# Kernel tuning notes

Measured on AMD Instinct MI355X. Metric: run time of the kernel, lower is better.

## Reference

```python
import jax, jax.numpy as jnp
import numpy as np

N = 50000        # nodes
E = 1_600_000    # edges per graph (avg degree 32)
T = 5            # timesteps per node
F_RAW = 395      # 3 meta channels + 392 signal
H_GRU = 64
HID = 40


def setup_inputs() -> dict:
    key = jax.random.key(0)
    ks = jax.random.split(key, 20)
    s = 0.05
    inp = {
        "x": jax.random.normal(ks[0], (N, T, F_RAW), jnp.float32),
        "edge_index": jax.random.randint(ks[1], (2, E), 0, N, dtype=jnp.int32),
        "feat_edge_index": jax.random.randint(ks[2], (2, E), 0, N, dtype=jnp.int32),
        # FeatureCNN: Conv1d(1, 16, kernel_size=40, stride=88) -> L=5 -> flatten 80
        "conv_w": jax.random.normal(ks[3], (16, 1, 40), jnp.float32) * s,
        "conv_b": jnp.zeros((16,), jnp.float32),
        "lin1_w": jax.random.normal(ks[4], (40, 80), jnp.float32) * s,
        "lin1_b": jnp.zeros((40,), jnp.float32),
        # GRU(input=41, hidden=64), PyTorch gate order: r, z, n
        "gru_w_ih": jax.random.normal(ks[5], (3 * H_GRU, 41), jnp.float32) * s,
        "gru_w_hh": jax.random.normal(ks[6], (3 * H_GRU, H_GRU), jnp.float32) * s,
        "gru_b_ih": jnp.zeros((3 * H_GRU,), jnp.float32),
        "gru_b_hh": jnp.zeros((3 * H_GRU,), jnp.float32),
        "gcn1_w": jax.random.normal(ks[7], (104, HID), jnp.float32) * s,
        "gcn1_b": jnp.zeros((HID,), jnp.float32),
        "gcn2_w": jax.random.normal(ks[8], (104, HID), jnp.float32) * s,
        "gcn2_b": jnp.zeros((HID,), jnp.float32),
        "mlp_w": jax.random.normal(ks[9], (1, 2 * HID), jnp.float32) * s,
        "mlp_b": jnp.zeros((1,), jnp.float32),
    }
    return inp


def _gcn(h_in, ei, W, b):
    """GCNConv: sym-normalized sum aggregation with self-loops."""
    n = h_in.shape[0]
    h = h_in @ W                                   # [n, out]
    loops = jnp.arange(n, dtype=ei.dtype)
    src = jnp.concatenate([ei[0], loops])
    dst = jnp.concatenate([ei[1], loops])
    deg = jax.ops.segment_sum(jnp.ones_like(dst, h.dtype), dst, num_segments=n)
    dinv = jax.lax.rsqrt(jnp.maximum(deg, 1.0))    # deg >= 1 due to self-loops
    norm = dinv[src] * dinv[dst]                   # [E+n]
    msg = h[src] * norm[:, None]                   # gather + scale
    return jax.ops.segment_sum(msg, dst, num_segments=n) + b


def _cnn_gru(x, conv_w, conv_b, lin1_w, lin1_b, gru_w_ih, gru_w_hh, gru_b_ih, gru_b_hh):
    n = x.shape[0]
    y = x[:, :, 2].reshape(-1, 1)                  # [n*5, 1]
    sig = x[:, :, 3:].reshape(-1, 1, 392)          # [n*5, 1, 392]
    # FeatureCNN: conv1d k=40 s=88 -> [n*5, 16, 5] -> relu -> flatten 80
    c = jax.lax.conv_general_dilated(
        sig, conv_w, window_strides=(88,), padding="VALID",
        dimension_numbers=("NCH", "OIH", "NCH"))
    c = jax.nn.relu(c + conv_b[None, :, None]).reshape(-1, 80)
    out = jax.nn.relu(c @ lin1_w.T + lin1_b)       # [n*5, 40]
    seq = jnp.concatenate([out, y], axis=1).reshape(n, 5, 41)

    def gru_step(h, xt):
        gi = xt @ gru_w_ih.T + gru_b_ih            # [n, 192]
        gh = h @ gru_w_hh.T + gru_b_hh
        ir, iz, inn = jnp.split(gi, 3, axis=1)
        hr, hz, hn_ = jnp.split(gh, 3, axis=1)
        r = jax.nn.sigmoid(ir + hr)
        z = jax.nn.sigmoid(iz + hz)
        ng = jnp.tanh(inn + r * hn_)
        h = (1.0 - z) * ng + z * h
        return h, None

    h0 = jnp.zeros((n, H_GRU), x.dtype)
    hn, _ = jax.lax.scan(gru_step, h0, jnp.swapaxes(seq[:, :4, :], 0, 1))
    return jnp.concatenate([seq[:, 4, :-1], hn], axis=1)  # [n, 104]


def reference(x, edge_index, feat_edge_index, conv_w, conv_b, lin1_w, lin1_b,
              gru_w_ih, gru_w_hh, gru_b_ih, gru_b_hh,
              gcn1_w, gcn1_b, gcn2_w, gcn2_b, mlp_w, mlp_b):
    feats = _cnn_gru(x, conv_w, conv_b, lin1_w, lin1_b,
                     gru_w_ih, gru_w_hh, gru_b_ih, gru_b_hh)   # [N, 104]
    emb1 = jax.nn.relu(_gcn(feats, edge_index, gcn1_w, gcn1_b))      # [N, 40]
    emb2 = jax.nn.relu(_gcn(feats, feat_edge_index, gcn2_w, gcn2_b)) # [N, 40]
    emb = jnp.concatenate([emb1, emb2], axis=1)                      # [N, 80]
    return emb @ mlp_w.T + mlp_b                                     # [N, 1]
```

## Files before the change

kernel.cpp:

```cpp
#include <hip/hip_runtime.h>
#include <hip/hip_fp16.h>
#include <math.h>


#define NB      512
#define MAXNPB  104
#define PART_T  4096
#define GN      96

__global__ __launch_bounds__(512) void k_cnn(
    const float* __restrict__ x,
    const float* __restrict__ conv_w,
    const float* __restrict__ conv_b,
    const float* __restrict__ lin_w,
    const float* __restrict__ lin_b,
    float* __restrict__ seq,
    float* __restrict__ feats,
    int nrows, int nnodes)
{
    __shared__ __align__(16) float smem[64 * 200];
    __shared__ __align__(16) float s_cw[16][44];
    __shared__ __align__(16) float s_lw[40][84];
    __shared__ float s_cb[16];
    __shared__ float s_lb[40];

    const int tid = threadIdx.x;
    const int r0  = blockIdx.x * 64;

    float sg[25];
    #pragma unroll
    for (int it = 0; it < 25; ++it) {
        int i = tid + it * 512;
        int row = i / 200, e = i - row * 200;
        int p = e / 40, kk = e - p * 40;
        int gr = r0 + row; if (gr >= nrows) gr = nrows - 1;
        sg[it] = x[(size_t)gr * 395 + 3 + 88 * p + kk];
    }

    for (int i = tid; i < 640;  i += 512) s_cw[i / 40][i % 40] = conv_w[i];
    for (int i = tid; i < 3200; i += 512) s_lw[i / 80][i % 80] = lin_w[i];
    if (tid < 16) s_cb[tid] = conv_b[tid];
    if (tid >= 64 && tid < 104) s_lb[tid - 64] = lin_b[tid - 64];

    if (tid < 64) {
        int gr = r0 + tid;
        if (gr < nrows) {
            float y = x[(size_t)gr * 395 + 2];
            int node = gr / 5, t = gr - node * 5;
            if (t < 4) seq[(t * nnodes + node) * 41 + 40] = y;
        }
    }

    #pragma unroll
    for (int it = 0; it < 25; ++it) {
        int i = tid + it * 512;
        int row = i / 200, e = i - row * 200;
        smem[row * 200 + e] = sg[it];
    }
    __syncthreads();

    const int row = tid >> 3, cg = tid & 7;
    float creg[2][5];
    {
        float acc[2][5];
        #pragma unroll
        for (int cc = 0; cc < 2; ++cc) {
            float b = s_cb[2 * cg + cc];
            #pragma unroll
            for (int p = 0; p < 5; ++p) acc[cc][p] = b;
        }
        #pragma unroll
        for (int k4 = 0; k4 < 40; k4 += 4) {
            float4 sv[5];
            #pragma unroll
            for (int p = 0; p < 5; ++p)
                sv[p] = *(const float4*)&smem[row * 200 + p * 40 + k4];
            #pragma unroll
            for (int cc = 0; cc < 2; ++cc) {
                float4 w4 = *(const float4*)&s_cw[2 * cg + cc][k4];
                #pragma unroll
                for (int p = 0; p < 5; ++p)
                    acc[cc][p] += w4.x * sv[p].x + w4.y * sv[p].y + w4.z * sv[p].z + w4.w * sv[p].w;
            }
        }
        #pragma unroll
        for (int cc = 0; cc < 2; ++cc)
            #pragma unroll
            for (int p = 0; p < 5; ++p) creg[cc][p] = fmaxf(acc[cc][p], 0.0f);
    }
    __syncthreads();

    #pragma unroll
    for (int cc = 0; cc < 2; ++cc)
        #pragma unroll
        for (int p = 0; p < 5; ++p)
            smem[row * 84 + (2 * cg + cc) * 5 + p] = creg[cc][p];
    __syncthreads();

    {
        const int jg = tid & 7;
        float acc[5];
        #pragma unroll
        for (int jj = 0; jj < 5; ++jj) acc[jj] = s_lb[5 * jg + jj];
        #pragma unroll
        for (int i4 = 0; i4 < 80; i4 += 4) {
            float4 c0 = *(const float4*)&smem[row * 84 + i4];
            #pragma unroll
            for (int jj = 0; jj < 5; ++jj) {
                float4 w4 = *(const float4*)&s_lw[5 * jg + jj][i4];
                acc[jj] += w4.x * c0.x + w4.y * c0.y + w4.z * c0.z + w4.w * c0.w;
            }
        }
        int gr = r0 + row;
        if (gr < nrows) {
            int node = gr / 5, t = gr - node * 5;
            #pragma unroll
            for (int jj = 0; jj < 5; ++jj) {
                float v = fmaxf(acc[jj], 0.0f);
                if (t < 4) seq[(t * nnodes + node) * 41 + 5 * jg + jj] = v;
                else       feats[node * 104 + 5 * jg + jj] = v;
            }
        }
    }
}

__global__ __launch_bounds__(512) void k_gru(
    const float* __restrict__ seq,
    const float* __restrict__ w_ih,
    const float* __restrict__ w_hh,
    const float* __restrict__ b_ih,
    const float* __restrict__ b_hh,
    float* __restrict__ feats,
    int nnodes)
{
    __shared__ __align__(16) __half s_wi[41][192];
    __shared__ __align__(16) __half s_wh[64][192];
    __shared__ __align__(16) float  s_h[64][104];
    __shared__ __align__(16) __half s_x[41][104];
    __shared__ float s_bi[192], s_bh[192];

    const int tid  = threadIdx.x;
    const int nblk = blockIdx.x * GN;

    float xr[8];
    #pragma unroll
    for (int r = 0; r < 8; ++r) {
        int i = tid + r * 512;
        if (i < GN * 41) {
            int nl = i / 41, k = i - nl * 41;
            int node = nblk + nl; if (node >= nnodes) node = nnodes - 1;
            xr[r] = seq[(size_t)node * 41 + k];
        }
    }

    for (int i = tid; i < 192 * 41; i += 512) { int g = i / 41, k = i - g * 41; s_wi[k][g] = __float2half(w_ih[i]); }
    for (int i = tid; i < 192 * 64; i += 512) { int g = i >> 6,  k = i & 63;    s_wh[k][g] = __float2half(w_hh[i]); }
    if (tid < 192) { s_bi[tid] = b_ih[tid]; s_bh[tid] = b_hh[tid]; }
    for (int i = tid; i < 64 * 104; i += 512) ((float*)s_h)[i] = 0.0f;

    #pragma unroll
    for (int r = 0; r < 8; ++r) {
        int i = tid + r * 512;
        if (i < GN * 41) { int nl = i / 41, k = i - nl * 41; s_x[k][nl] = __float2half(xr[r]); }
    }
    __syncthreads();

    const int jg = tid & 31, ngp = tid >> 5;
    const int j0 = 2 * jg, n0 = 6 * ngp;

    float hreg[2][6];
    #pragma unroll
    for (int a = 0; a < 2; ++a)
        #pragma unroll
        for (int b = 0; b < 6; ++b) hreg[a][b] = 0.0f;

    for (int t = 0; t < 4; ++t) {
        if (t < 3) {
            #pragma unroll
            for (int r = 0; r < 8; ++r) {
                int i = tid + r * 512;
                if (i < GN * 41) {
                    int nl = i / 41, k = i - nl * 41;
                    int node = nblk + nl; if (node >= nnodes) node = nnodes - 1;
                    xr[r] = seq[(size_t)((t + 1) * nnodes + node) * 41 + k];
                }
            }
        }

        float ar[2][6], az[2][6], ani[2][6], anh[2][6];
        #pragma unroll
        for (int a = 0; a < 2; ++a)
            #pragma unroll
            for (int b = 0; b < 6; ++b) { ar[a][b]=0.f; az[a][b]=0.f; ani[a][b]=0.f; anh[a][b]=0.f; }

        for (int k = 0; k < 41; ++k) {
            float2 x01 = __half22float2(*(const __half2*)&s_x[k][n0]);
            float2 x23 = __half22float2(*(const __half2*)&s_x[k][n0 + 2]);
            float2 x45 = __half22float2(*(const __half2*)&s_x[k][n0 + 4]);
            float xv[6] = {x01.x, x01.y, x23.x, x23.y, x45.x, x45.y};
            float2 wr = __half22float2(*(const __half2*)&s_wi[k][j0]);
            float2 wz = __half22float2(*(const __half2*)&s_wi[k][64 + j0]);
            float2 wn = __half22float2(*(const __half2*)&s_wi[k][128 + j0]);
            #pragma unroll
            for (int nn = 0; nn < 6; ++nn) {
                ar[0][nn] += wr.x*xv[nn]; ar[1][nn] += wr.y*xv[nn];
                az[0][nn] += wz.x*xv[nn]; az[1][nn] += wz.y*xv[nn];
                ani[0][nn]+= wn.x*xv[nn]; ani[1][nn]+= wn.y*xv[nn];
            }
        }
        for (int k = 0; k < 64; ++k) {
            float2 h01 = *(const float2*)&s_h[k][n0];
            float2 h23 = *(const float2*)&s_h[k][n0 + 2];
            float2 h45 = *(const float2*)&s_h[k][n0 + 4];
            float hv[6] = {h01.x, h01.y, h23.x, h23.y, h45.x, h45.y};
            float2 wr = __half22float2(*(const __half2*)&s_wh[k][j0]);
            float2 wz = __half22float2(*(const __half2*)&s_wh[k][64 + j0]);
            float2 wn = __half22float2(*(const __half2*)&s_wh[k][128 + j0]);
            #pragma unroll
            for (int nn = 0; nn < 6; ++nn) {
                ar[0][nn] += wr.x*hv[nn]; ar[1][nn] += wr.y*hv[nn];
                az[0][nn] += wz.x*hv[nn]; az[1][nn] += wz.y*hv[nn];
                anh[0][nn]+= wn.x*hv[nn]; anh[1][nn]+= wn.y*hv[nn];
            }
        }

        #pragma unroll
        for (int jj = 0; jj < 2; ++jj) {
            int j = j0 + jj;
            float br  = s_bi[j]      + s_bh[j];
            float bz  = s_bi[64 + j] + s_bh[64 + j];
            float bin = s_bi[128 + j], bhn = s_bh[128 + j];
            #pragma unroll
            for (int nn = 0; nn < 6; ++nn) {
                float r = 1.0f / (1.0f + expf(-(ar[jj][nn] + br)));
                float z = 1.0f / (1.0f + expf(-(az[jj][nn] + bz)));
                float g = tanhf(ani[jj][nn] + bin + r * (anh[jj][nn] + bhn));
                hreg[jj][nn] = (1.0f - z) * g + z * hreg[jj][nn];
            }
        }
        __syncthreads();

        if (t < 3) {
            #pragma unroll
            for (int jj = 0; jj < 2; ++jj) {
                *(float2*)&s_h[j0 + jj][n0]     = make_float2(hreg[jj][0], hreg[jj][1]);
                *(float2*)&s_h[j0 + jj][n0 + 2] = make_float2(hreg[jj][2], hreg[jj][3]);
                *(float2*)&s_h[j0 + jj][n0 + 4] = make_float2(hreg[jj][4], hreg[jj][5]);
            }
            #pragma unroll
            for (int r = 0; r < 8; ++r) {
                int i = tid + r * 512;
                if (i < GN * 41) { int nl = i / 41, k = i - nl * 41; s_x[k][nl] = __float2half(xr[r]); }
            }
            __syncthreads();
        }
    }

    #pragma unroll
    for (int jj = 0; jj < 2; ++jj)
        #pragma unroll
        for (int nn = 0; nn < 6; ++nn) {
            int node = nblk + n0 + nn;
            if (node < nnodes) feats[node * 104 + 40 + j0 + jj] = hreg[jj][nn];
        }
}

__global__ __launch_bounds__(256) void k_hw(
    const float* __restrict__ feats,
    const float* __restrict__ w1,
    const float* __restrict__ w2,
    const float* __restrict__ dinv1,
    const float* __restrict__ dinv2,
    __half* __restrict__ hs1,
    __half* __restrict__ hs2,
    int nnodes)
{
    __shared__ __align__(16) float s_f[128][108];
    __shared__ __align__(16) float s_w[80][108];
    __shared__ float s_d[2][128];

    const int tid  = threadIdx.x;
    const int nblk = blockIdx.x * 128;

    for (int i = tid; i < 128 * 104; i += 256) {
        int n = i / 104, k = i - n * 104;
        int node = nblk + n; if (node >= nnodes) node = nnodes - 1;
        s_f[n][k] = feats[node * 104 + k];
    }
    for (int i = tid; i < 80 * 104; i += 256) {
        int o = i / 104, k = i - o * 104;
        s_w[o][k] = (o < 40) ? w1[k * 40 + o] : w2[k * 40 + (o - 40)];
    }
    if (tid < 128) {
        int node = nblk + tid; if (node >= nnodes) node = nnodes - 1;
        s_d[0][tid] = dinv1[node]; s_d[1][tid] = dinv2[node];
    }
    __syncthreads();

    const int og = tid & 7, ngp = tid >> 3;
    const int o0 = 10 * og, n0 = 4 * ngp;
    float acc[4][10];
    #pragma unroll
    for (int a = 0; a < 4; ++a)
        #pragma unroll
        for (int b = 0; b < 10; ++b) acc[a][b] = 0.0f;

    for (int k4 = 0; k4 < 104; k4 += 4) {
        float4 f[4];
        #pragma unroll
        for (int nn = 0; nn < 4; ++nn) f[nn] = *(const float4*)&s_f[n0 + nn][k4];
        #pragma unroll
        for (int oo = 0; oo < 10; ++oo) {
            float4 w4 = *(const float4*)&s_w[o0 + oo][k4];
            #pragma unroll
            for (int nn = 0; nn < 4; ++nn)
                acc[nn][oo] += w4.x * f[nn].x + w4.y * f[nn].y + w4.z * f[nn].z + w4.w * f[nn].w;
        }
    }
    #pragma unroll
    for (int nn = 0; nn < 4; ++nn) {
        int node = nblk + n0 + nn;
        if (node >= nnodes) continue;
        #pragma unroll
        for (int oo = 0; oo < 10; oo += 2) {
            int o = o0 + oo;
            float dscale = (o < 40) ? s_d[0][n0 + nn] : s_d[1][n0 + nn];
            __half2 h2 = __floats2half2_rn(dscale * acc[nn][oo], dscale * acc[nn][oo + 1]);
            if (o < 40) *(__half2*)&hs1[node * 40 + o]        = h2;
            else        *(__half2*)&hs2[node * 40 + (o - 40)] = h2;
        }
    }
}

__global__ void k_zero2(int* a, int* b, int n) {
    int i = blockIdx.x * 256 + threadIdx.x;
    if (i < n) { a[i] = 0; b[i] = 0; }
}

__global__ void k_deg(const int* __restrict__ d1, const int* __restrict__ d2,
                      int* c1, int* c2, int E) {
    int i = blockIdx.x * 256 + threadIdx.x;
    if (i < E) { atomicAdd(&c1[d1[i]], 1); atomicAdd(&c2[d2[i]], 1); }
}

__global__ __launch_bounds__(1024) void k_scan2(
    const int* __restrict__ cnt1, int* __restrict__ roff1, float* __restrict__ dinv1,
    const int* __restrict__ cnt2, int* __restrict__ roff2, float* __restrict__ dinv2,
    int* __restrict__ bcur, int npb, int n)
{
    const int* cnt  = blockIdx.x ? cnt2  : cnt1;
    int*       roff = blockIdx.x ? roff2 : roff1;
    float*     dinv = blockIdx.x ? dinv2 : dinv1;
    int*       bc   = bcur + (blockIdx.x ? NB : 0);

    __shared__ int sp[1024];
    int t = threadIdx.x;
    int C = (n + 1023) >> 10;
    int i0 = t * C, i1 = min(i0 + C, n);
    int s = 0;
    for (int i = i0; i < i1; ++i) s += cnt[i];
    sp[t] = s;
    __syncthreads();
    for (int off = 1; off < 1024; off <<= 1) {
        int v = (t >= off) ? sp[t - off] : 0;
        __syncthreads();
        sp[t] += v;
        __syncthreads();
    }
    int run = sp[t] - s;
    for (int i = i0; i < i1; ++i) {
        int c = cnt[i];
        roff[i] = run;
        dinv[i] = rsqrtf((float)(c + 1));
        run += c;
    }
    if (t == 1023) roff[n] = sp[1023];
    __syncthreads();
    if (t < NB) {
        int lo = min(t * npb, n);
        bc[t] = roff[lo];
    }
}

__global__ __launch_bounds__(256) void k_part(
    const int* __restrict__ e,
    int* __restrict__ bcur,
    unsigned long long* __restrict__ pairs,
    int E, int npb)
{
    __shared__ unsigned long long s_ed[PART_T];
    __shared__ int s_cnt[NB], s_base[NB], s_cur[NB];
    const int tid = threadIdx.x;
    const int e0  = blockIdx.x * PART_T;
    const int ne  = min(PART_T, E - e0);

    for (int i = tid; i < NB; i += 256) { s_cnt[i] = 0; s_cur[i] = 0; }
    __syncthreads();

    for (int k = tid; k < ne; k += 256) {
        int s = e[e0 + k], d = e[E + e0 + k];
        s_ed[k] = ((unsigned long long)(unsigned)d << 32) | (unsigned)s;
        atomicAdd(&s_cnt[d / npb], 1);
    }
    __syncthreads();
    for (int b = tid; b < NB; b += 256)
        if (s_cnt[b] > 0) s_base[b] = atomicAdd(&bcur[b], s_cnt[b]);
    __syncthreads();
    for (int k = tid; k < ne; k += 256) {
        unsigned long long p = s_ed[k];
        int b = (int)(p >> 32) / npb;
        int r = atomicAdd(&s_cur[b], 1);
        pairs[s_base[b] + r] = p;
    }
}

__global__ __launch_bounds__(256) void k_scatter3(
    const unsigned long long* __restrict__ pairs,
    const int* __restrict__ roff, int* __restrict__ csr,
    int n, int npb)
{
    __shared__ int s_cur[MAXNPB];
    const int tid = threadIdx.x;
    const int b   = blockIdx.x;
    const int lo  = b * npb;
    if (lo >= n) return;
    const int hi = min(lo + npb, n);
    const int nd = hi - lo;

    for (int i = tid; i < nd; i += 256) s_cur[i] = roff[lo + i];
    __syncthreads();

    const int seg0 = roff[lo], seg1 = roff[hi];
    for (int p = seg0 + tid; p < seg1; p += 256) {
        unsigned long long pr = pairs[p];
        int d = (int)(pr >> 32), s = (int)(pr & 0xffffffffu);
        int pos = atomicAdd(&s_cur[d - lo], 1);
        csr[pos] = s;
    }
}

__global__ __launch_bounds__(512) void k_agg(
    const __half* __restrict__ hs, const int* __restrict__ csr,
    const int* __restrict__ roff, const float* __restrict__ dinv,
    const float* __restrict__ bias, const float* __restrict__ mw,
    const float* __restrict__ mlp_b, float* __restrict__ out,
    int n, int accumulate)
{
    int wv = threadIdx.x >> 6, lane = threadIdx.x & 63;
    int d = blockIdx.x * 8 + wv;
    if (d >= n) return;
    int beg = roff[d], end = roff[d + 1];
    int fc = lane < 40 ? lane : 0;
    float acc = 0.0f;
    int e = beg;
    for (; e + 8 <= end; e += 8) {
        int s0 = csr[e],     s1 = csr[e + 1], s2 = csr[e + 2], s3 = csr[e + 3];
        int s4 = csr[e + 4], s5 = csr[e + 5], s6 = csr[e + 6], s7 = csr[e + 7];
        float a0 = __half2float(hs[(size_t)s0 * 40 + fc]);
        float a1 = __half2float(hs[(size_t)s1 * 40 + fc]);
        float a2 = __half2float(hs[(size_t)s2 * 40 + fc]);
        float a3 = __half2float(hs[(size_t)s3 * 40 + fc]);
        float a4 = __half2float(hs[(size_t)s4 * 40 + fc]);
        float a5 = __half2float(hs[(size_t)s5 * 40 + fc]);
        float a6 = __half2float(hs[(size_t)s6 * 40 + fc]);
        float a7 = __half2float(hs[(size_t)s7 * 40 + fc]);
        acc += ((a0 + a1) + (a2 + a3)) + ((a4 + a5) + (a6 + a7));
    }
    for (; e < end; ++e) acc += __half2float(hs[(size_t)csr[e] * 40 + fc]);

    float v = dinv[d] * (__half2float(hs[(size_t)d * 40 + fc]) + acc) + bias[fc];
    v = fmaxf(v, 0.0f) * mw[fc];
    if (lane >= 40) v = 0.0f;
    #pragma unroll
    for (int off = 32; off > 0; off >>= 1) v += __shfl_down(v, off);
    if (lane == 0)
        out[d] = accumulate ? (out[d] + v) : (mlp_b[0] + v);
}

extern "C" void kernel_launch(void* const* d_in, const int* in_sizes, int n_in,
                              void* d_out, int out_size, void* d_ws, size_t ws_size,
                              hipStream_t stream)
{
    const float* x      = (const float*)d_in[0];
    const int*   ei1    = (const int*)d_in[1];
    const int*   ei2    = (const int*)d_in[2];
    const float* conv_w = (const float*)d_in[3];
    const float* conv_b = (const float*)d_in[4];
    const float* lin_w  = (const float*)d_in[5];
    const float* lin_b  = (const float*)d_in[6];
    const float* w_ih   = (const float*)d_in[7];
    const float* w_hh   = (const float*)d_in[8];
    const float* b_ih   = (const float*)d_in[9];
    const float* b_hh   = (const float*)d_in[10];
    const float* g1w    = (const float*)d_in[11];
    const float* g1b    = (const float*)d_in[12];
    const float* g2w    = (const float*)d_in[13];
    const float* g2b    = (const float*)d_in[14];
    const float* mw     = (const float*)d_in[15];
    const float* mb     = (const float*)d_in[16];

    const int N = in_sizes[0] / (5 * 395);
    const int E = in_sizes[1] / 2;
    const int R = N * 5;
    float* out = (float*)d_out;

    const int npb = (N + NB - 1) / NB;
    if (npb > MAXNPB) return;

    char* wp = (char*)d_ws;
    auto alloc = [&](size_t bytes) {
        char* p = wp; wp += (bytes + 255) & ~(size_t)255; return p;
    };
    size_t seq_bytes = (size_t)4 * N * 41 * 4;
    float*  seq   = (float*)alloc(seq_bytes);
    float*  feats = (float*)alloc((size_t)N * 104 * 4);
    __half* hs1   = (__half*)alloc((size_t)N * 40 * 2);
    __half* hs2   = (__half*)alloc((size_t)N * 40 * 2);
    int*    csr1  = (int*)alloc((size_t)E * 4);
    int*    csr2  = (int*)alloc((size_t)E * 4);
    int*    cnt1  = (int*)alloc((size_t)N * 4);
    int*    cnt2  = (int*)alloc((size_t)N * 4);
    int*    roff1 = (int*)alloc((size_t)(N + 1) * 4);
    int*    roff2 = (int*)alloc((size_t)(N + 1) * 4);
    float*  dinv1 = (float*)alloc((size_t)N * 4);
    float*  dinv2 = (float*)alloc((size_t)N * 4);
    int*    bcur  = (int*)alloc((size_t)2 * NB * 4);

    unsigned long long *pairs1, *pairs2;
    if (2 * (size_t)E * 8 <= seq_bytes) {
        pairs1 = (unsigned long long*)seq;
        pairs2 = pairs1 + E;
    } else {
        pairs1 = (unsigned long long*)alloc((size_t)E * 8);
        pairs2 = (unsigned long long*)alloc((size_t)E * 8);
    }
    if ((size_t)(wp - (char*)d_ws) > ws_size) return;

    hipLaunchKernelGGL(k_zero2,    dim3((N + 255) / 256), dim3(256), 0, stream, cnt1, cnt2, N);
    hipLaunchKernelGGL(k_deg,      dim3((E + 255) / 256), dim3(256), 0, stream, ei1 + E, ei2 + E, cnt1, cnt2, E);
    hipLaunchKernelGGL(k_scan2,    dim3(2), dim3(1024), 0, stream, cnt1, roff1, dinv1, cnt2, roff2, dinv2, bcur, npb, N);
    hipLaunchKernelGGL(k_part,     dim3((E + PART_T - 1) / PART_T), dim3(256), 0, stream, ei1, bcur,      pairs1, E, npb);
    hipLaunchKernelGGL(k_part,     dim3((E + PART_T - 1) / PART_T), dim3(256), 0, stream, ei2, bcur + NB, pairs2, E, npb);
    hipLaunchKernelGGL(k_scatter3, dim3(NB), dim3(256), 0, stream, pairs1, roff1, csr1, N, npb);
    hipLaunchKernelGGL(k_scatter3, dim3(NB), dim3(256), 0, stream, pairs2, roff2, csr2, N, npb);
    hipLaunchKernelGGL(k_cnn,      dim3((R + 63) / 64), dim3(512), 0, stream, x, conv_w, conv_b, lin_w, lin_b, seq, feats, R, N);
    hipLaunchKernelGGL(k_gru,      dim3((N + GN - 1) / GN), dim3(512), 0, stream, seq, w_ih, w_hh, b_ih, b_hh, feats, N);
    hipLaunchKernelGGL(k_hw,       dim3((N + 127) / 128), dim3(256), 0, stream, feats, g1w, g2w, dinv1, dinv2, hs1, hs2, N);
    hipLaunchKernelGGL(k_agg,      dim3((N + 7) / 8), dim3(512), 0, stream, hs1, csr1, roff1, dinv1, g1b, mw,      mb, out, N, 0);
    hipLaunchKernelGGL(k_agg,      dim3((N + 7) / 8), dim3(512), 0, stream, hs2, csr2, roff2, dinv2, g2b, mw + 40, mb, out, N, 1);
}
```

Before: 824.9 us.

## Rewrite GRU kernel as one-thread-per-node with register hidden state

```diff
diff --git a/kernel.cpp b/kernel.cpp
--- a/kernel.cpp
+++ b/kernel.cpp
@@ -6,7 +6,6 @@
 #define NB      512
 #define MAXNPB  104
 #define PART_T  4096
-#define GN      96
 
 __global__ __launch_bounds__(512) void k_cnn(
     const float* __restrict__ x,
@@ -124,7 +123,7 @@
     }
 }
 
-__global__ __launch_bounds__(512) void k_gru(
+__global__ __launch_bounds__(128) void k_gru(
     const float* __restrict__ seq,
     const float* __restrict__ w_ih,
     const float* __restrict__ w_hh,
@@ -133,136 +132,59 @@
     float* __restrict__ feats,
     int nnodes)
 {
-    __shared__ __align__(16) __half s_wi[41][192];
-    __shared__ __align__(16) __half s_wh[64][192];
-    __shared__ __align__(16) float  s_h[64][104];
-    __shared__ __align__(16) __half s_x[41][104];
-    __shared__ float s_bi[192], s_bh[192];
-
+    __shared__ float s_a[128][66];
+    __shared__ float s_z[128][66];
     const int tid  = threadIdx.x;
-    const int nblk = blockIdx.x * GN;
-
-    float xr[8];
-    #pragma unroll
-    for (int r = 0; r < 8; ++r) {
-        int i = tid + r * 512;
-        if (i < GN * 41) {
-            int nl = i / 41, k = i - nl * 41;
-            int node = nblk + nl; if (node >= nnodes) node = nnodes - 1;
-            xr[r] = seq[(size_t)node * 41 + k];
-        }
-    }
-
-    for (int i = tid; i < 192 * 41; i += 512) { int g = i / 41, k = i - g * 41; s_wi[k][g] = __float2half(w_ih[i]); }
-    for (int i = tid; i < 192 * 64; i += 512) { int g = i >> 6,  k = i & 63;    s_wh[k][g] = __float2half(w_hh[i]); }
-    if (tid < 192) { s_bi[tid] = b_ih[tid]; s_bh[tid] = b_hh[tid]; }
-    for (int i = tid; i < 64 * 104; i += 512) ((float*)s_h)[i] = 0.0f;
-
-    #pragma unroll
-    for (int r = 0; r < 8; ++r) {
-        int i = tid + r * 512;
-        if (i < GN * 41) { int nl = i / 41, k = i - nl * 41; s_x[k][nl] = __float2half(xr[r]); }
-    }
-    __syncthreads();
-
-    const int jg = tid & 31, ngp = tid >> 5;
-    const int j0 = 2 * jg, n0 = 6 * ngp;
-
-    float hreg[2][6];
-    #pragma unroll
-    for (int a = 0; a < 2; ++a)
-        #pragma unroll
-        for (int b = 0; b < 6; ++b) hreg[a][b] = 0.0f;
+    const int node = blockIdx.x * 128 + tid;
+    const int nc   = node < nnodes ? node : nnodes - 1;
+
+    float h[64];
+    #pragma unroll
+    for (int k = 0; k < 64; ++k) h[k] = 0.0f;
 
     for (int t = 0; t < 4; ++t) {
-        if (t < 3) {
-            #pragma unroll
-            for (int r = 0; r < 8; ++r) {
-                int i = tid + r * 512;
-                if (i < GN * 41) {
-                    int nl = i / 41, k = i - nl * 41;
-                    int node = nblk + nl; if (node >= nnodes) node = nnodes - 1;
-                    xr[r] = seq[(size_t)((t + 1) * nnodes + node) * 41 + k];
-                }
+        float x[41];
+        const float* xr = seq + ((size_t)t * nnodes + nc) * 41;
+        #pragma unroll
+        for (int k = 0; k < 41; ++k) x[k] = xr[k];
+
+        for (int j = 0; j < 64; ++j) {
+            const float* wr = w_ih + j * 41;
+            const float* wz = w_ih + (64 + j) * 41;
+            const float* wn = w_ih + (128 + j) * 41;
+            float ar = b_ih[j], az = b_ih[64 + j], an = b_ih[128 + j];
+            #pragma unroll
+            for (int k = 0; k < 41; ++k) {
+                ar += x[k] * wr[k];
+                az += x[k] * wz[k];
+                an += x[k] * wn[k];
             }
-        }
-
-        float ar[2][6], az[2][6], ani[2][6], anh[2][6];
-        #pragma unroll
-        for (int a = 0; a < 2; ++a)
-            #pragma unroll
-            for (int b = 0; b < 6; ++b) { ar[a][b]=0.f; az[a][b]=0.f; ani[a][b]=0.f; anh[a][b]=0.f; }
-
-        for (int k = 0; k < 41; ++k) {
-            float2 x01 = __half22float2(*(const __half2*)&s_x[k][n0]);
-            float2 x23 = __half22float2(*(const __half2*)&s_x[k][n0 + 2]);
-            float2 x45 = __half22float2(*(const __half2*)&s_x[k][n0 + 4]);
-            float xv[6] = {x01.x, x01.y, x23.x, x23.y, x45.x, x45.y};
-            float2 wr = __half22float2(*(const __half2*)&s_wi[k][j0]);
-            float2 wz = __half22float2(*(const __half2*)&s_wi[k][64 + j0]);
-            float2 wn = __half22float2(*(const __half2*)&s_wi[k][128 + j0]);
-            #pragma unroll
-            for (int nn = 0; nn < 6; ++nn) {
-                ar[0][nn] += wr.x*xv[nn]; ar[1][nn] += wr.y*xv[nn];
-                az[0][nn] += wz.x*xv[nn]; az[1][nn] += wz.y*xv[nn];
-                ani[0][nn]+= wn.x*xv[nn]; ani[1][nn]+= wn.y*xv[nn];
+            const float* vr = w_hh + j * 64;
+            const float* vz = w_hh + (64 + j) * 64;
+            const float* vn = w_hh + (128 + j) * 64;
+            float hr = b_hh[j], hz = b_hh[64 + j], hn_ = b_hh[128 + j];
+            #pragma unroll
+            for (int k = 0; k < 64; ++k) {
+                hr  += h[k] * vr[k];
+                hz  += h[k] * vz[k];
+                hn_ += h[k] * vn[k];
             }
-        }
-        for (int k = 0; k < 64; ++k) {
-            float2 h01 = *(const float2*)&s_h[k][n0];
-            float2 h23 = *(const float2*)&s_h[k][n0 + 2];
-            float2 h45 = *(const float2*)&s_h[k][n0 + 4];
-            float hv[6] = {h01.x, h01.y, h23.x, h23.y, h45.x, h45.y};
-            float2 wr = __half22float2(*(const __half2*)&s_wh[k][j0]);
-            float2 wz = __half22float2(*(const __half2*)&s_wh[k][64 + j0]);
-            float2 wn = __half22float2(*(const __half2*)&s_wh[k][128 + j0]);
-            #pragma unroll
-            for (int nn = 0; nn < 6; ++nn) {
-                ar[0][nn] += wr.x*hv[nn]; ar[1][nn] += wr.y*hv[nn];
-                az[0][nn] += wz.x*hv[nn]; az[1][nn] += wz.y*hv[nn];
-                anh[0][nn]+= wn.x*hv[nn]; anh[1][nn]+= wn.y*hv[nn];
-            }
-        }
-
-        #pragma unroll
-        for (int jj = 0; jj < 2; ++jj) {
-            int j = j0 + jj;
-            float br  = s_bi[j]      + s_bh[j];
-            float bz  = s_bi[64 + j] + s_bh[64 + j];
-            float bin = s_bi[128 + j], bhn = s_bh[128 + j];
-            #pragma unroll
-            for (int nn = 0; nn < 6; ++nn) {
-                float r = 1.0f / (1.0f + expf(-(ar[jj][nn] + br)));
-                float z = 1.0f / (1.0f + expf(-(az[jj][nn] + bz)));
-                float g = tanhf(ani[jj][nn] + bin + r * (anh[jj][nn] + bhn));
-                hreg[jj][nn] = (1.0f - z) * g + z * hreg[jj][nn];
-            }
-        }
-        __syncthreads();
-
-        if (t < 3) {
-            #pragma unroll
-            for (int jj = 0; jj < 2; ++jj) {
-                *(float2*)&s_h[j0 + jj][n0]     = make_float2(hreg[jj][0], hreg[jj][1]);
-                *(float2*)&s_h[j0 + jj][n0 + 2] = make_float2(hreg[jj][2], hreg[jj][3]);
-                *(float2*)&s_h[j0 + jj][n0 + 4] = make_float2(hreg[jj][4], hreg[jj][5]);
-            }
-            #pragma unroll
-            for (int r = 0; r < 8; ++r) {
-                int i = tid + r * 512;
-                if (i < GN * 41) { int nl = i / 41, k = i - nl * 41; s_x[k][nl] = __float2half(xr[r]); }
-            }
-            __syncthreads();
-        }
-    }
-
-    #pragma unroll
-    for (int jj = 0; jj < 2; ++jj)
-        #pragma unroll
-        for (int nn = 0; nn < 6; ++nn) {
-            int node = nblk + n0 + nn;
-            if (node < nnodes) feats[node * 104 + 40 + j0 + jj] = hreg[jj][nn];
-        }
+            float r = 1.0f / (1.0f + expf(-(ar + hr)));
+            float z = 1.0f / (1.0f + expf(-(az + hz)));
+            float g = tanhf(an + r * hn_);
+            s_a[tid][j] = (1.0f - z) * g;
+            s_z[tid][j] = z;
+        }
+        #pragma unroll
+        for (int j = 0; j < 64; ++j)
+            h[j] = s_a[tid][j] + s_z[tid][j] * h[j];
+    }
+
+    if (node < nnodes) {
+        #pragma unroll
+        for (int j = 0; j < 64; ++j)
+            feats[node * 104 + 40 + j] = h[j];
+    }
 }
 
 __global__ __launch_bounds__(256) void k_hw(
@@ -544,7 +466,7 @@
     hipLaunchKernelGGL(k_scatter3, dim3(NB), dim3(256), 0, stream, pairs1, roff1, csr1, N, npb);
     hipLaunchKernelGGL(k_scatter3, dim3(NB), dim3(256), 0, stream, pairs2, roff2, csr2, N, npb);
     hipLaunchKernelGGL(k_cnn,      dim3((R + 63) / 64), dim3(512), 0, stream, x, conv_w, conv_b, lin_w, lin_b, seq, feats, R, N);
-    hipLaunchKernelGGL(k_gru,      dim3((N + GN - 1) / GN), dim3(512), 0, stream, seq, w_ih, w_hh, b_ih, b_hh, feats, N);
+    hipLaunchKernelGGL(k_gru,      dim3((N + 127) / 128), dim3(128), 0, stream, seq, w_ih, w_hh, b_ih, b_hh, feats, N);
     hipLaunchKernelGGL(k_hw,       dim3((N + 127) / 128), dim3(256), 0, stream, feats, g1w, g2w, dinv1, dinv2, hs1, hs2, N);
     hipLaunchKernelGGL(k_agg,      dim3((N + 7) / 8), dim3(512), 0, stream, hs1, csr1, roff1, dinv1, g1b, mw,      mb, out, N, 0);
     hipLaunchKernelGGL(k_agg,      dim3((N + 7) / 8), dim3(512), 0, stream, hs2, csr2, roff2, dinv2, g2b, mw + 40, mb, out, N, 1);
```

Result: slower. 1.293 ms (+56.8%).
